# Optimization experiments

Hardware: AMD Instinct MI355X
Metric: run time of the kernel (lower is better)

## Reference

```python
import jax, jax.numpy as jnp
import numpy as np

DYADIC_LEVELS = 3
SIG_LEVEL = 3  # hardcoded depth-3 truncated signature (matches init_kwargs)


def path_signature(inc):
    """Truncated (level-3) path signature of a piecewise-linear path.

    inc: [..., N, d] increments. Returns [..., d + d^2 + d^3] flattened
    signature (levels 1..3, row-major tensor flattening, no scalar term),
    computed via Chen's relation: S <- S (x) exp(dx).
    """
    d = inc.shape[-1]
    bshape = inc.shape[:-2]
    inc_t = jnp.moveaxis(inc, -2, 0)  # [N, ..., d]
    s1 = jnp.zeros(bshape + (d,), inc.dtype)
    s2 = jnp.zeros(bshape + (d, d), inc.dtype)
    s3 = jnp.zeros(bshape + (d, d, d), inc.dtype)

    def step(carry, dx):
        s1, s2, s3 = carry
        dx2 = dx[..., :, None] * dx[..., None, :]          # dx (x) dx
        dx3 = dx2[..., :, :, None] * dx[..., None, None, :]
        n3 = (s3
              + s2[..., :, :, None] * dx[..., None, None, :]
              + 0.5 * s1[..., :, None, None] * dx2[..., None, :, :]
              + dx3 / 6.0)
        n2 = s2 + s1[..., :, None] * dx[..., None, :] + 0.5 * dx2
        n1 = s1 + dx
        return (n1, n2, n3), None

    (s1, s2, s3), _ = jax.lax.scan(step, (s1, s2, s3), inc_t)
    return jnp.concatenate(
        [s1, s2.reshape(bshape + (d * d,)), s3.reshape(bshape + (d * d * d,))],
        axis=-1)


def setup_inputs() -> dict:
    key = jax.random.key(0)
    x = jax.random.normal(key, (64, 1024, 64, 4), dtype=jnp.float32)
    return {"x": x}


def reference(x):
    # x: [batch, frame, element, coords] -> [batch, element, pieces, terms]
    B, T, E, D = x.shape
    xr = jnp.transpose(x, (0, 2, 1, 3))  # [B, E, T, D]
    pieces = []
    for lvl in range(DYADIC_LEVELS + 1):
        P = 2 ** lvl
        L = T // P  # frames per dyadic piece (T divisible by 2**DYADIC_LEVELS)
        xp = xr.reshape(B, E, P, L, D)
        inc = jnp.diff(xp, axis=3)  # [B, E, P, L-1, D]; signatory uses x[start:end]
        pieces.append(path_signature(inc))  # [B, E, P, terms]
    return jnp.concatenate(pieces, axis=2)  # [B, E, 15, 84]
```

## Files before the change

### kernel.cpp

```cpp
#include <hip/hip_runtime.h>

#define DEV __device__ __forceinline__


DEV void async_stage16(const void* gsrc, void* ldst) {
    __builtin_amdgcn_global_load_lds(
        (const __attribute__((address_space(1))) unsigned int*)gsrc,
        (__attribute__((address_space(3))) unsigned int*)ldst, 16, 0, 0);
}

DEV void sig_step(float s1[4], float s2[16], float s3[64], const float dx[4]) {
    float h[4], u[4], g[4];
#pragma unroll
    for (int j = 0; j < 4; ++j) {
        h[j] = 0.5f * dx[j];
        u[j] = fmaf(dx[j], (1.0f / 3.0f), s1[j]);
        g[j] = s1[j] + h[j];
    }
#pragma unroll
    for (int i = 0; i < 4; ++i)
#pragma unroll
        for (int j = 0; j < 4; ++j) {
            float t = fmaf(u[i], h[j], s2[i * 4 + j]);
#pragma unroll
            for (int k = 0; k < 4; ++k)
                s3[i * 16 + j * 4 + k] = fmaf(t, dx[k], s3[i * 16 + j * 4 + k]);
        }
#pragma unroll
    for (int i = 0; i < 4; ++i)
#pragma unroll
        for (int j = 0; j < 4; ++j)
            s2[i * 4 + j] = fmaf(g[i], dx[j], s2[i * 4 + j]);
#pragma unroll
    for (int i = 0; i < 4; ++i) s1[i] += dx[i];
}

DEV void sig_init(float s1[4], float s2[16], float s3[64], const float dx[4]) {
#pragma unroll
    for (int i = 0; i < 4; ++i) s1[i] = dx[i];
#pragma unroll
    for (int j = 0; j < 4; ++j) {
        float hj = 0.5f * dx[j];
#pragma unroll
        for (int k = 0; k < 4; ++k) s2[j * 4 + k] = hj * dx[k];
    }
#pragma unroll
    for (int i = 0; i < 4; ++i) {
        float ti = dx[i] * (1.0f / 3.0f);
#pragma unroll
        for (int jk = 0; jk < 16; ++jk) s3[i * 16 + jk] = ti * s2[jk];
    }
}

DEV void chen_fold(float a1[4], float a2[16], float a3[64], const float* __restrict__ b) {
    float b1[4], b2[16];
#pragma unroll
    for (int k = 0; k < 4; ++k) b1[k] = b[k * 64];
#pragma unroll
    for (int t = 0; t < 16; ++t) b2[t] = b[(4 + t) * 64];
#pragma unroll
    for (int i = 0; i < 4; ++i)
#pragma unroll
        for (int j = 0; j < 4; ++j)
#pragma unroll
            for (int k = 0; k < 4; ++k) {
                float v = a3[i * 16 + j * 4 + k] + b[(20 + i * 16 + j * 4 + k) * 64];
                v = fmaf(a2[i * 4 + j], b1[k], v);
                v = fmaf(a1[i], b2[j * 4 + k], v);
                a3[i * 16 + j * 4 + k] = v;
            }
#pragma unroll
    for (int i = 0; i < 4; ++i)
#pragma unroll
        for (int j = 0; j < 4; ++j)
            a2[i * 4 + j] = fmaf(a1[i], b1[j], a2[i * 4 + j] + b2[i * 4 + j]);
#pragma unroll
    for (int i = 0; i < 4; ++i) a1[i] += b1[i];
}

DEV void store_sig(float* dst, const float s1[4], const float s2[16], const float s3[64]) {
#pragma unroll
    for (int t = 0; t < 4; ++t) dst[t * 64] = s1[t];
#pragma unroll
    for (int t = 0; t < 16; ++t) dst[(4 + t) * 64] = s2[t];
#pragma unroll
    for (int t = 0; t < 64; ++t) dst[(20 + t) * 64] = s3[t];
}

DEV void load_sig(const float* src, float s1[4], float s2[16], float s3[64]) {
#pragma unroll
    for (int t = 0; t < 4; ++t) s1[t] = src[t * 64];
#pragma unroll
    for (int t = 0; t < 16; ++t) s2[t] = src[(4 + t) * 64];
#pragma unroll
    for (int t = 0; t < 64; ++t) s3[t] = src[(20 + t) * 64];
}

DEV void write_out(float* ob, const float s1[4], const float s2[16], const float s3[64]) {
#pragma unroll
    for (int t = 0; t < 4; ++t) ob[t] = s1[t];
#pragma unroll
    for (int t = 0; t < 16; ++t) ob[4 + t] = s2[t];
#pragma unroll
    for (int t = 0; t < 64; ++t) ob[20 + t] = s3[t];
}

__global__ __attribute__((amdgpu_flat_work_group_size(256, 256),
                          amdgpu_waves_per_eu(2, 2)))
void half_kernel(const float* __restrict__ x, float* __restrict__ hsig,
                 float* __restrict__ bdxh) {
    __shared__ float lds[16384];
    float4* lf = reinterpret_cast<float4*>(lds);
    const int b = blockIdx.x >> 4;
    const int h = blockIdx.x & 15;
    const int w = threadIdx.x >> 6;
    const int e = threadIdx.x & 63;
    const float4* xg4 = reinterpret_cast<const float4*>(x) + (long)b * 65536;
    const int fbase = h * 64;

#pragma unroll
    for (int k = 0; k < 16; ++k) {
        const int f = w * 16 + k;
        async_stage16(xg4 + (long)(fbase + f) * 64 + e, &lf[f * 64]);
    }
    if (w == 0 && h > 0) {
        float4 pm = xg4[(long)(fbase - 1) * 64 + e];
        float4 p0 = xg4[(long)fbase * 64 + e];
        float* bb = &bdxh[(((long)(b * 16 + h)) * 4) * 64 + e];
        bb[0]   = p0.x - pm.x;
        bb[64]  = p0.y - pm.y;
        bb[128] = p0.z - pm.z;
        bb[192] = p0.w - pm.w;
    }
    asm volatile("s_waitcnt vmcnt(0)" ::: "memory");
    __syncthreads();

    const int base = w * 16;
    const int NI = (w < 3) ? 16 : 15;
    float s1[4], s2[16], s3[64];
    float dxx[4];
#define DX_(a, c) { dxx[0] = c.x - a.x; dxx[1] = c.y - a.y; \
                    dxx[2] = c.z - a.z; dxx[3] = c.w - a.w; }
    float4 a = lf[base * 64 + e];
    float4 nx = lf[(base + 1) * 64 + e];
    DX_(a, nx); sig_init(s1, s2, s3, dxx);
    a = nx;
    nx = lf[(base + 2) * 64 + e];
#pragma unroll 1
    for (int j = 2; j <= NI; ++j) {
        float4 cu = nx;
        int jn = j + 1; jn = jn > NI ? NI : jn;
        nx = lf[(base + jn) * 64 + e];
        DX_(a, cu); sig_step(s1, s2, s3, dxx);
        a = cu;
    }
#undef DX_
    __syncthreads();

    float* slot0 = &lds[0];
    float* slot1 = &lds[84 * 64];
    if (w == 1) store_sig(slot0 + e, s1, s2, s3);
    if (w == 3) store_sig(slot1 + e, s1, s2, s3);
    __syncthreads();
    if (w == 0) chen_fold(s1, s2, s3, slot0 + e);
    if (w == 2) chen_fold(s1, s2, s3, slot1 + e);
    __syncthreads();
    if (w == 2) store_sig(slot0 + e, s1, s2, s3);
    __syncthreads();
    if (w == 0) {
        chen_fold(s1, s2, s3, slot0 + e);
        store_sig(&hsig[(((long)(b * 16 + h)) * 84) * 64 + e], s1, s2, s3);
    }
}

__global__ __attribute__((amdgpu_flat_work_group_size(128, 128),
                          amdgpu_waves_per_eu(1, 1)))
void quad_kernel(const float* __restrict__ hsig, const float* __restrict__ bdxh,
                 float* __restrict__ qsig, float* __restrict__ out) {
    __shared__ float slot[84 * 64];
    const int b = blockIdx.x >> 2;
    const int q = blockIdx.x & 3;
    const int w = threadIdx.x >> 6;
    const int e = threadIdx.x & 63;
    const int h0 = q * 4 + w * 2;

    float s1[4], s2[16], s3[64];
    load_sig(&hsig[(((long)(b * 16 + h0)) * 84) * 64 + e], s1, s2, s3);
    {
        const float* bb = &bdxh[(((long)(b * 16 + h0 + 1)) * 4) * 64 + e];
        float dx[4] = {bb[0], bb[64], bb[128], bb[192]};
        sig_step(s1, s2, s3, dx);
        chen_fold(s1, s2, s3, &hsig[(((long)(b * 16 + h0 + 1)) * 84) * 64 + e]);
    }
    write_out(&out[(((long)(b * 64 + e)) * 15 + 7 + 2 * q + w) * 84], s1, s2, s3);

    if (w == 1) store_sig(&slot[e], s1, s2, s3);
    __syncthreads();
    if (w == 0) {
        const float* bb = &bdxh[(((long)(b * 16 + q * 4 + 2)) * 4) * 64 + e];
        float dx[4] = {bb[0], bb[64], bb[128], bb[192]};
        sig_step(s1, s2, s3, dx);
        chen_fold(s1, s2, s3, &slot[e]);
        store_sig(&qsig[(((long)(b * 4 + q)) * 84) * 64 + e], s1, s2, s3);
        write_out(&out[(((long)(b * 64 + e)) * 15 + 3 + q) * 84], s1, s2, s3);
    }
}

__global__ __attribute__((amdgpu_flat_work_group_size(128, 128),
                          amdgpu_waves_per_eu(1, 1)))
void final_kernel(const float* __restrict__ qsig, const float* __restrict__ bdxh,
                  float* __restrict__ out) {
    __shared__ float slot[84 * 64];
    const int b = blockIdx.x;
    const int w = threadIdx.x >> 6;
    const int e = threadIdx.x & 63;

    float s1[4], s2[16], s3[64];
    const int q0 = w * 2;
    load_sig(&qsig[(((long)(b * 4 + q0)) * 84) * 64 + e], s1, s2, s3);
    {
        const int hb = (w == 0) ? 4 : 12;
        const float* bb = &bdxh[(((long)(b * 16 + hb)) * 4) * 64 + e];
        float dx[4] = {bb[0], bb[64], bb[128], bb[192]};
        sig_step(s1, s2, s3, dx);
        chen_fold(s1, s2, s3, &qsig[(((long)(b * 4 + q0 + 1)) * 84) * 64 + e]);
    }
    write_out(&out[(((long)(b * 64 + e)) * 15 + 1 + w) * 84], s1, s2, s3);

    if (w == 1) store_sig(&slot[e], s1, s2, s3);
    __syncthreads();
    if (w == 0) {
        const float* bb = &bdxh[(((long)(b * 16 + 8)) * 4) * 64 + e];
        float dx[4] = {bb[0], bb[64], bb[128], bb[192]};
        sig_step(s1, s2, s3, dx);
        chen_fold(s1, s2, s3, &slot[e]);
        write_out(&out[(((long)(b * 64 + e)) * 15 + 0) * 84], s1, s2, s3);
    }
}

__global__ __attribute__((amdgpu_flat_work_group_size(64, 64),
                          amdgpu_waves_per_eu(1, 1)))
void direct_kernel(const float* __restrict__ x, float* __restrict__ out) {
    const int pg = blockIdx.x % 15;
    const int b = blockIdx.x / 15;
    const int e = threadIdx.x;
    int lvl, p;
    if (pg == 0)      { lvl = 0; p = 0; }
    else if (pg < 3)  { lvl = 1; p = pg - 1; }
    else if (pg < 7)  { lvl = 2; p = pg - 3; }
    else              { lvl = 3; p = pg - 7; }
    const int L = 1024 >> lvl;
    const int t0 = p * L;
    const float4* xf = reinterpret_cast<const float4*>(x);
    const long base = (long)b * 65536;

    float4 prev = xf[base + (long)t0 * 64 + e];
    float s1[4], s2[16], s3[64];
    {
        float4 cur = xf[base + (long)(t0 + 1) * 64 + e];
        float dx[4] = {cur.x - prev.x, cur.y - prev.y, cur.z - prev.z, cur.w - prev.w};
        sig_init(s1, s2, s3, dx);
        prev = cur;
    }
    for (int i = 2; i < L; ++i) {
        float4 cur = xf[base + (long)(t0 + i) * 64 + e];
        float dx[4] = {cur.x - prev.x, cur.y - prev.y, cur.z - prev.z, cur.w - prev.w};
        prev = cur;
        sig_step(s1, s2, s3, dx);
    }
    write_out(&out[(((long)(b * 64 + e)) * 15 + pg) * 84], s1, s2, s3);
}

extern "C" void kernel_launch(void* const* d_in, const int* in_sizes, int n_in,
                              void* d_out, int out_size, void* d_ws, size_t ws_size,
                              hipStream_t stream) {
    (void)in_sizes; (void)n_in; (void)out_size;
    const float* x = (const float*)d_in[0];
    float* out = (float*)d_out;

    const size_t h_elems = (size_t)64 * 16 * 84 * 64;
    const size_t b_elems = (size_t)64 * 16 * 4 * 64;
    const size_t q_elems = (size_t)64 * 4 * 84 * 64;
    const size_t need = (h_elems + b_elems + q_elems) * sizeof(float);

    if (ws_size >= need) {
        float* hsig = (float*)d_ws;
        float* bdxh = hsig + h_elems;
        float* qsig = bdxh + b_elems;
        half_kernel<<<64 * 16, 256, 0, stream>>>(x, hsig, bdxh);
        quad_kernel<<<64 * 4, 128, 0, stream>>>(hsig, bdxh, qsig, out);
        final_kernel<<<64, 128, 0, stream>>>(qsig, bdxh, out);
    } else {
        direct_kernel<<<64 * 15, 64, 0, stream>>>(x, out);
    }
}
```

Baseline: 48.37 us.

## Drop block barrier via per-wave halo staging; vectorize output stores

Each wave now stages its own boundary frame into LDS (waves 0-2 load one extra frame), so the block-wide barrier after the async loads can be removed and each wave waits only on its own loads. Output writes switch from scalar stores to float4 stores, since each output row of 84 floats is 16-byte aligned. Launch attributes move to __launch_bounds__, which raises the allowed occupancy for the quad and final kernels. The shared frame is now loaded twice, and vmcnt-only waiting relies on each wave reading only LDS it staged itself.

```diff
diff --git a/kernel.cpp b/kernel.cpp
--- a/kernel.cpp
+++ b/kernel.cpp
@@ -96,17 +96,18 @@
     for (int t = 0; t < 64; ++t) s3[t] = src[(20 + t) * 64];
 }
 
-DEV void write_out(float* ob, const float s1[4], const float s2[16], const float s3[64]) {
-#pragma unroll
-    for (int t = 0; t < 4; ++t) ob[t] = s1[t];
-#pragma unroll
-    for (int t = 0; t < 16; ++t) ob[4 + t] = s2[t];
-#pragma unroll
-    for (int t = 0; t < 64; ++t) ob[20 + t] = s3[t];
-}
-
-__global__ __attribute__((amdgpu_flat_work_group_size(256, 256),
-                          amdgpu_waves_per_eu(2, 2)))
+DEV void write_out4(float* ob, const float s1[4], const float s2[16], const float s3[64]) {
+    float4* o4 = reinterpret_cast<float4*>(ob);
+    o4[0] = make_float4(s1[0], s1[1], s1[2], s1[3]);
+#pragma unroll
+    for (int t = 0; t < 4; ++t)
+        o4[1 + t] = make_float4(s2[4 * t], s2[4 * t + 1], s2[4 * t + 2], s2[4 * t + 3]);
+#pragma unroll
+    for (int t = 0; t < 16; ++t)
+        o4[5 + t] = make_float4(s3[4 * t], s3[4 * t + 1], s3[4 * t + 2], s3[4 * t + 3]);
+}
+
+__global__ __launch_bounds__(256, 2)
 void half_kernel(const float* __restrict__ x, float* __restrict__ hsig,
                  float* __restrict__ bdxh) {
     __shared__ float lds[16384];
@@ -119,9 +120,11 @@
     const int fbase = h * 64;
 
 #pragma unroll
-    for (int k = 0; k < 16; ++k) {
-        const int f = w * 16 + k;
-        async_stage16(xg4 + (long)(fbase + f) * 64 + e, &lf[f * 64]);
+    for (int k = 0; k < 17; ++k) {
+        if (k < 16 || w < 3) {
+            const int f = w * 16 + k;
+            async_stage16(xg4 + (long)(fbase + f) * 64 + e, &lf[f * 64]);
+        }
     }
     if (w == 0 && h > 0) {
         float4 pm = xg4[(long)(fbase - 1) * 64 + e];
@@ -133,7 +136,6 @@
         bb[192] = p0.w - pm.w;
     }
     asm volatile("s_waitcnt vmcnt(0)" ::: "memory");
-    __syncthreads();
 
     const int base = w * 16;
     const int NI = (w < 3) ? 16 : 15;
@@ -173,8 +175,7 @@
     }
 }
 
-__global__ __attribute__((amdgpu_flat_work_group_size(128, 128),
-                          amdgpu_waves_per_eu(1, 1)))
+__global__ __launch_bounds__(128, 2)
 void quad_kernel(const float* __restrict__ hsig, const float* __restrict__ bdxh,
                  float* __restrict__ qsig, float* __restrict__ out) {
     __shared__ float slot[84 * 64];
@@ -192,7 +193,7 @@
         sig_step(s1, s2, s3, dx);
         chen_fold(s1, s2, s3, &hsig[(((long)(b * 16 + h0 + 1)) * 84) * 64 + e]);
     }
-    write_out(&out[(((long)(b * 64 + e)) * 15 + 7 + 2 * q + w) * 84], s1, s2, s3);
+    write_out4(&out[(((long)(b * 64 + e)) * 15 + 7 + 2 * q + w) * 84], s1, s2, s3);
 
     if (w == 1) store_sig(&slot[e], s1, s2, s3);
     __syncthreads();
@@ -202,12 +203,11 @@
         sig_step(s1, s2, s3, dx);
         chen_fold(s1, s2, s3, &slot[e]);
         store_sig(&qsig[(((long)(b * 4 + q)) * 84) * 64 + e], s1, s2, s3);
-        write_out(&out[(((long)(b * 64 + e)) * 15 + 3 + q) * 84], s1, s2, s3);
-    }
-}
-
-__global__ __attribute__((amdgpu_flat_work_group_size(128, 128),
-                          amdgpu_waves_per_eu(1, 1)))
+        write_out4(&out[(((long)(b * 64 + e)) * 15 + 3 + q) * 84], s1, s2, s3);
+    }
+}
+
+__global__ __launch_bounds__(128, 2)
 void final_kernel(const float* __restrict__ qsig, const float* __restrict__ bdxh,
                   float* __restrict__ out) {
     __shared__ float slot[84 * 64];
@@ -225,7 +225,7 @@
         sig_step(s1, s2, s3, dx);
         chen_fold(s1, s2, s3, &qsig[(((long)(b * 4 + q0 + 1)) * 84) * 64 + e]);
     }
-    write_out(&out[(((long)(b * 64 + e)) * 15 + 1 + w) * 84], s1, s2, s3);
+    write_out4(&out[(((long)(b * 64 + e)) * 15 + 1 + w) * 84], s1, s2, s3);
 
     if (w == 1) store_sig(&slot[e], s1, s2, s3);
     __syncthreads();
@@ -234,12 +234,11 @@
         float dx[4] = {bb[0], bb[64], bb[128], bb[192]};
         sig_step(s1, s2, s3, dx);
         chen_fold(s1, s2, s3, &slot[e]);
-        write_out(&out[(((long)(b * 64 + e)) * 15 + 0) * 84], s1, s2, s3);
-    }
-}
-
-__global__ __attribute__((amdgpu_flat_work_group_size(64, 64),
-                          amdgpu_waves_per_eu(1, 1)))
+        write_out4(&out[(((long)(b * 64 + e)) * 15 + 0) * 84], s1, s2, s3);
+    }
+}
+
+__global__ __launch_bounds__(64, 1)
 void direct_kernel(const float* __restrict__ x, float* __restrict__ out) {
     const int pg = blockIdx.x % 15;
     const int b = blockIdx.x / 15;
@@ -268,7 +267,7 @@
         prev = cur;
         sig_step(s1, s2, s3, dx);
     }
-    write_out(&out[(((long)(b * 64 + e)) * 15 + pg) * 84], s1, s2, s3);
+    write_out4(&out[(((long)(b * 64 + e)) * 15 + pg) * 84], s1, s2, s3);
 }
 
 extern "C" void kernel_launch(void* const* d_in, const int* in_sizes, int n_in,
```

Result: no change. 48.28 us (-0.2%).
